# Kernel optimization log

Hardware: AMD Instinct MI355X
Metric: run time of the kernel (lower is better)

Reference implementation:

```python
import jax, jax.numpy as jnp
import numpy as np
import math

D_EMBED = 1024
N_HEADS = 16
HEAD_DIM = D_EMBED // N_HEADS
ROPE_BASE = 10000.0


def apply_rope(x):
    # x: [B, S, H, D] ; torchtune-style interleaved RoPE
    B, S, H, D = x.shape
    half = D // 2
    inv_freq = 1.0 / (ROPE_BASE ** (jnp.arange(0, D, 2, dtype=jnp.float32) / D))  # [half]
    angles = jnp.arange(S, dtype=jnp.float32)[:, None] * inv_freq[None, :]        # [S, half]
    cos = jnp.cos(angles)[None, :, None, :].astype(x.dtype)  # [1,S,1,half]
    sin = jnp.sin(angles)[None, :, None, :].astype(x.dtype)
    x1 = x[..., 0::2]
    x2 = x[..., 1::2]
    o1 = x1 * cos - x2 * sin
    o2 = x1 * sin + x2 * cos
    return jnp.stack([o1, o2], axis=-1).reshape(B, S, H, D)


def setup_inputs() -> dict:
    key = jax.random.key(0)
    ks = jax.random.split(key, 7)
    B, S = 4, 2048
    d_tri = D_EMBED
    q = jax.random.normal(ks[0], (B, S, 2 * d_tri), dtype=jnp.float32)
    k = jax.random.normal(ks[1], (B, S, 2 * d_tri), dtype=jnp.float32)
    v = jax.random.normal(ks[2], (B, S, d_tri), dtype=jnp.float32)
    s_in = 1.0 / math.sqrt(2 * d_tri)
    s_tri = 1.0 / math.sqrt(d_tri)
    W_q = jax.random.normal(ks[3], (D_EMBED, 2 * d_tri), dtype=jnp.float32) * s_in
    W_k = jax.random.normal(ks[4], (D_EMBED, 2 * d_tri), dtype=jnp.float32) * s_in
    W_v = jax.random.normal(ks[5], (d_tri, d_tri), dtype=jnp.float32) * s_tri
    W_o = jax.random.normal(ks[6], (d_tri, d_tri), dtype=jnp.float32) * s_tri
    return {"q": q, "k": k, "v": v, "W_q": W_q, "W_k": W_k, "W_v": W_v, "W_o": W_o}


def reference(q, k, v, W_q, W_k, W_v, W_o):
    B, S, _ = q.shape
    H, Dh = N_HEADS, HEAD_DIM
    scale = 1.0 / math.sqrt(D_EMBED)

    qp = (q @ W_q.T).reshape(B, S, H, Dh)
    kp = (k @ W_k.T).reshape(B, S, H, Dh)
    vp = (v @ W_v.T).reshape(B, S, H, Dh)

    qp = apply_rope(qp)
    kp = apply_rope(kp)

    # [B,H,S,S]
    scores = jnp.einsum('bqhd,bkhd->bhqk', qp, kp) * scale
    causal = jnp.tril(jnp.ones((S, S), dtype=bool))
    scores = jnp.where(causal[None, None], scores, -jnp.inf)
    probs = jax.nn.softmax(scores, axis=-1)
    # dropout layers are identity in eval mode
    out = jnp.einsum('bhqk,bkhd->bqhd', probs, vp).reshape(B, S, D_EMBED)
    return out @ W_o.T
```

## Files before the change

### kernel.cpp

```cpp
#include <hip/hip_runtime.h>
#include <math.h>

#define S_LEN 2048
#define DEMB  1024
#define DH    64

typedef short bf16x8 __attribute__((ext_vector_type(8)));
typedef short bf16x4 __attribute__((ext_vector_type(4)));
typedef float floatx4 __attribute__((ext_vector_type(4)));

__device__ __forceinline__ short f2bf(float f) {
    unsigned u = __builtin_bit_cast(unsigned, f);
    u += 0x7FFFu + ((u >> 16) & 1u);
    return (short)(u >> 16);
}

__global__ void rope_table_k(float2* __restrict__ tab) {
    int idx = blockIdx.x * 256 + threadIdx.x;
    int s = idx >> 5, i = idx & 31;
    double ang = (double)s * pow(10000.0, -(double)i / 32.0);
    tab[idx] = make_float2((float)cos(ang), (float)sin(ang));
}

struct CvtArgs { const float* src[7]; short* dst[7]; int n[7]; };
__global__ __launch_bounds__(256) void cvt_k(CvtArgs a) {
    int seg = blockIdx.y;
    int idx = (blockIdx.x * 256 + threadIdx.x) * 8;
    if (idx >= a.n[seg]) return;
    const float4* s = (const float4*)(a.src[seg] + idx);
    float4 v0 = s[0], v1 = s[1];
    bf16x8 r;
    r[0] = f2bf(v0.x); r[1] = f2bf(v0.y); r[2] = f2bf(v0.z); r[3] = f2bf(v0.w);
    r[4] = f2bf(v1.x); r[5] = f2bf(v1.y); r[6] = f2bf(v1.z); r[7] = f2bf(v1.w);
    *(bf16x8*)(a.dst[seg] + idx) = r;
}

__device__ __forceinline__ void gld16(const void* g, void* l) {
    __builtin_amdgcn_global_load_lds(
        (const __attribute__((address_space(1))) void*)g,
        (__attribute__((address_space(3))) void*)l, 16, 0, 0);
}

template<int EPI>
__device__ __forceinline__ void gemm_body(
    const short* __restrict__ A, const short* __restrict__ B,
    void* __restrict__ Cout, const float2* __restrict__ rope_tab,
    int K, short* smem)
{
    short* sA = smem;
    short* sB = smem + 8192;

    const int tid  = threadIdx.x;
    const int lane = tid & 63;
    const int wv   = tid >> 6;
    const int wm   = wv >> 1, wn = wv & 1;
    const int lr   = lane & 15, quad = lane >> 4;
    const int m0   = blockIdx.y * 128, n0 = blockIdx.x * 128;
    const int N    = 1024;

    const short* gA[4]; const short* gB[4];
    #pragma unroll
    for (int j = 0; j < 4; j++) {
        int c = j * 256 + tid;
        int row = c >> 3, sp = c & 7;
        int cs = (sp ^ (row & 7)) * 8;
        gA[j] = A + (size_t)(m0 + row) * K + cs;
        gB[j] = B + (size_t)(n0 + row) * K + cs;
    }

    floatx4 acc[4][4] = {};

    for (int k0 = 0; k0 < K; k0 += 64) {
        #pragma unroll
        for (int j = 0; j < 4; j++) {
            gld16(gA[j] + k0, sA + j * 2048 + wv * 512);
            gld16(gB[j] + k0, sB + j * 2048 + wv * 512);
        }
        __syncthreads();
        bf16x8 af[4][2], bfr[4][2];
        #pragma unroll
        for (int t = 0; t < 4; t++)
            #pragma unroll
            for (int ks = 0; ks < 2; ks++) {
                int ph = (ks * 4 + quad) ^ (lr & 7);
                af[t][ks]  = *reinterpret_cast<const bf16x8*>(&sA[(wm * 64 + t * 16 + lr) * 64 + ph * 8]);
                bfr[t][ks] = *reinterpret_cast<const bf16x8*>(&sB[(wn * 64 + t * 16 + lr) * 64 + ph * 8]);
            }
        #pragma unroll
        for (int ks = 0; ks < 2; ks++)
            #pragma unroll
            for (int mt = 0; mt < 4; mt++)
                #pragma unroll
                for (int nt = 0; nt < 4; nt++)
                    acc[mt][nt] = __builtin_amdgcn_mfma_f32_16x16x32_bf16(af[mt][ks], bfr[nt][ks], acc[mt][nt], 0, 0, 0);
        __syncthreads();
    }

    if constexpr (EPI == 0) {
        unsigned* sTi = (unsigned*)smem;
        #pragma unroll
        for (int nt = 0; nt < 4; nt++) {
            int n_l = wn * 64 + nt * 16 + lr;
            int ii  = ((n0 + n_l) & 63) >> 1;
            #pragma unroll
            for (int mt = 0; mt < 4; mt++)
                #pragma unroll
                for (int r = 0; r < 4; r++) {
                    int row_l = wm * 64 + mt * 16 + quad * 4 + r;
                    float2 cs = rope_tab[((m0 + row_l) & (S_LEN - 1)) * 32 + ii];
                    float v  = acc[mt][nt][r];
                    float vn = __shfl_xor(v, 1);
                    float o0 = v * cs.x - vn * cs.y;
                    float o1 = vn * cs.x + v * cs.y;
                    if (!(lr & 1)) {
                        unsigned pk = (unsigned)(unsigned short)f2bf(o0) |
                                      ((unsigned)(unsigned short)f2bf(o1) << 16);
                        sTi[row_l * 68 + (n_l >> 1)] = pk;
                    }
                }
        }
        __syncthreads();
        short* C = (short*)Cout;
        #pragma unroll
        for (int j = 0; j < 8; j++) {
            int c = j * 256 + tid;
            int row = c >> 4, col = (c & 15) * 8;
            bf16x8 val = *reinterpret_cast<const bf16x8*>(&smem[row * 136 + col]);
            *reinterpret_cast<bf16x8*>(&C[(size_t)(m0 + row) * N + n0 + col]) = val;
        }
    } else if constexpr (EPI == 2) {
        float* C = (float*)Cout;
        #pragma unroll
        for (int mt = 0; mt < 4; mt++)
            #pragma unroll
            for (int r = 0; r < 4; r++) {
                size_t rowoff = (size_t)(m0 + wm * 64 + mt * 16 + quad * 4 + r) * N;
                #pragma unroll
                for (int nt = 0; nt < 4; nt++)
                    C[rowoff + n0 + wn * 64 + nt * 16 + lr] = acc[mt][nt][r];
            }
    } else {
        short* sT = smem;
        #pragma unroll
        for (int nt = 0; nt < 4; nt++) {
            int nl = wn * 64 + nt * 16 + lr;
            #pragma unroll
            for (int mt = 0; mt < 4; mt++)
                #pragma unroll
                for (int r = 0; r < 4; r++)
                    sT[nl * 136 + wm * 64 + mt * 16 + quad * 4 + r] = f2bf(acc[mt][nt][r]);
        }
        __syncthreads();
        short* C = (short*)Cout;
        int bb = m0 >> 11;
        int s_base = m0 & (S_LEN - 1);
        #pragma unroll
        for (int i = 0; i < 8; i++) {
            int col = (tid >> 4) + i * 16;
            int mc  = (tid & 15) * 8;
            bf16x8 v = *reinterpret_cast<const bf16x8*>(&sT[col * 136 + mc]);
            size_t row = (size_t)bb * DEMB + (n0 + col);
            *reinterpret_cast<bf16x8*>(&C[row * S_LEN + s_base + mc]) = v;
        }
    }
}

__global__ __launch_bounds__(256, 3) void gemm_proj(
    const short* __restrict__ Aq, const short* __restrict__ Bq, void* __restrict__ Cq,
    const short* __restrict__ Ak, const short* __restrict__ Bk, void* __restrict__ Ck,
    const short* __restrict__ Av, const short* __restrict__ Bv, void* __restrict__ Cv,
    const float2* __restrict__ rope_tab)
{
    __shared__ __align__(16) short smem[17408];
    if (blockIdx.z == 0)
        gemm_body<0>(Aq, Bq, Cq, rope_tab, 2048, smem);
    else if (blockIdx.z == 1)
        gemm_body<0>(Ak, Bk, Ck, rope_tab, 2048, smem);
    else
        gemm_body<1>(Av, Bv, Cv, nullptr, 1024, smem);
}

__global__ __launch_bounds__(256, 3) void gemm_out(
    const short* __restrict__ A, const short* __restrict__ B, void* __restrict__ Cout)
{
    __shared__ __align__(16) short smem[17408];
    gemm_body<2>(A, B, Cout, nullptr, 1024, smem);
}

__global__ __launch_bounds__(256, 3) void flash_k(
    const short* __restrict__ qp, const short* __restrict__ kp,
    const short* __restrict__ vpT, short* __restrict__ attn)
{
    __shared__ __align__(16) short sKV[2][2][4096];
    __shared__ __align__(16) short sPb[4][2048];

    const int tid = threadIdx.x;
    const int w = tid >> 6, lane = tid & 63, lr = lane & 15, quad = lane >> 4;
    const int qt = 15 - (blockIdx.x >> 6);
    const int bh = blockIdx.x & 63;
    const int b = bh >> 4, h = bh & 15;
    const int R = qt * 128 + w * 32;
    const size_t qbase = (size_t)(b * S_LEN) * DEMB + h * DH;

    const short* kbase = kp + qbase;
    const short* vbase = vpT + ((size_t)(b * DEMB) + h * DH) * S_LEN;

    const int srow = tid >> 3;
    const int sp   = tid & 7;
    const int cs   = (sp ^ (srow & 7)) * 8;
    short* dK0 = &sKV[0][0][w * 512];  short* dV0 = &sKV[0][1][w * 512];
    short* dK1 = &sKV[1][0][w * 512];  short* dV1 = &sKV[1][1][w * 512];

    bf16x8 qf[2][2];
    #pragma unroll
    for (int mt = 0; mt < 2; mt++)
        #pragma unroll
        for (int ks = 0; ks < 2; ks++)
            qf[mt][ks] = *reinterpret_cast<const bf16x8*>(
                &qp[qbase + (size_t)(R + mt * 16 + lr) * DEMB + ks * 32 + quad * 8]);

    floatx4 oacc[2][4] = {};
    float lsum[2][4] = {};
    const float CEXP = 0.045084220081510574f;
    short* pw = sPb[w];

    const int ktend = 2 * qt + 1;

    auto stage = [&](int kt, int buf) {
        const short* kg = kbase + (size_t)kt * 64 * DEMB;
        const short* vg = vbase + kt * 64;
        short* dK = buf ? dK1 : dK0;
        short* dV = buf ? dV1 : dV0;
        gld16(kg + (size_t)srow * DEMB + cs,        dK);
        gld16(kg + (size_t)(srow + 32) * DEMB + cs, dK + 2048);
        gld16(vg + (size_t)srow * S_LEN + cs,       dV);
        gld16(vg + (size_t)(srow + 32) * S_LEN + cs, dV + 2048);
    };

    stage(0, 0);
    __syncthreads();

    for (int kt = 0; kt <= ktend; kt++) {
        const int cur = kt & 1;
        if (kt < ktend) stage(kt + 1, cur ^ 1);

        if (R + 31 >= kt * 64) {
            const short* sK = sKV[cur][0];
            const short* sV = sKV[cur][1];

            bf16x8 kf[4][2], vf[4][2];
            #pragma unroll
            for (int nt = 0; nt < 4; nt++)
                #pragma unroll
                for (int ks = 0; ks < 2; ks++) {
                    int ph = (ks * 4 + quad) ^ (lr & 7);
                    kf[nt][ks] = *reinterpret_cast<const bf16x8*>(&sK[(nt * 16 + lr) * 64 + ph * 8]);
                    vf[nt][ks] = *reinterpret_cast<const bf16x8*>(&sV[(nt * 16 + lr) * 64 + ph * 8]);
                }

            floatx4 st[2][4];
            #pragma unroll
            for (int nt = 0; nt < 4; nt++)
                #pragma unroll
                for (int mt = 0; mt < 2; mt++) {
                    floatx4 z = {};
                    z = __builtin_amdgcn_mfma_f32_16x16x32_bf16(qf[mt][0], kf[nt][0], z, 0, 0, 0);
                    st[mt][nt] = __builtin_amdgcn_mfma_f32_16x16x32_bf16(qf[mt][1], kf[nt][1], z, 0, 0, 0);
                }

            const bool need_mask = (kt * 64 + 63 > R);
            #pragma unroll
            for (int mt = 0; mt < 2; mt++)
                #pragma unroll
                for (int nt = 0; nt < 4; nt++)
                    #pragma unroll
                    for (int r = 0; r < 4; r++) {
                        float t = fminf(st[mt][nt][r] * CEXP, 80.f);
                        float p = __builtin_amdgcn_exp2f(t);
                        if (need_mask) {
                            int col = kt * 64 + nt * 16 + lr;
                            int row = R + mt * 16 + quad * 4 + r;
                            p = (col > row) ? 0.f : p;
                        }
                        st[mt][nt][r] = p;
                        lsum[mt][r] += p;
                    }

            #pragma unroll
            for (int mt = 0; mt < 2; mt++)
                #pragma unroll
                for (int nt = 0; nt < 4; nt++)
                    #pragma unroll
                    for (int r = 0; r < 4; r++) {
                        int rw = mt * 16 + quad * 4 + r;
                        int chunk = (nt * 2 + (lr >> 3)) ^ (rw & 7);
                        pw[rw * 64 + chunk * 8 + (lr & 7)] = f2bf(st[mt][nt][r]);
                    }

            bf16x8 pf[2][2];
            #pragma unroll
            for (int mt = 0; mt < 2; mt++)
                #pragma unroll
                for (int ks = 0; ks < 2; ks++) {
                    int rr = mt * 16 + lr;
                    int c  = (ks * 4 + quad) ^ (rr & 7);
                    pf[mt][ks] = *reinterpret_cast<const bf16x8*>(&pw[rr * 64 + c * 8]);
                }

            #pragma unroll
            for (int d = 0; d < 4; d++)
                #pragma unroll
                for (int mt = 0; mt < 2; mt++) {
                    oacc[mt][d] = __builtin_amdgcn_mfma_f32_16x16x32_bf16(pf[mt][0], vf[d][0], oacc[mt][d], 0, 0, 0);
                    oacc[mt][d] = __builtin_amdgcn_mfma_f32_16x16x32_bf16(pf[mt][1], vf[d][1], oacc[mt][d], 0, 0, 0);
                }
        }
        __syncthreads();
    }

    #pragma unroll
    for (int mt = 0; mt < 2; mt++)
        #pragma unroll
        for (int r = 0; r < 4; r++) {
            float l = lsum[mt][r];
            l += __shfl_xor(l, 1);
            l += __shfl_xor(l, 2);
            l += __shfl_xor(l, 4);
            l += __shfl_xor(l, 8);
            float inv = 1.f / l;
            size_t rowoff = qbase + (size_t)(R + mt * 16 + quad * 4 + r) * DEMB;
            #pragma unroll
            for (int d = 0; d < 4; d++)
                attn[rowoff + d * 16 + lr] = f2bf(oacc[mt][d][r] * inv);
        }
}

__device__ __forceinline__ bf16x4 load4(const float* p) {
    const float4 v = *reinterpret_cast<const float4*>(p);
    bf16x4 r; r[0] = f2bf(v.x); r[1] = f2bf(v.y); r[2] = f2bf(v.z); r[3] = f2bf(v.w);
    return r;
}
__device__ __forceinline__ bf16x4 load4(const short* p) {
    return *reinterpret_cast<const bf16x4*>(p);
}

template<typename TA, int EPI>
__global__ __launch_bounds__(256) void gemm_nt(
    const TA* __restrict__ A, const float* __restrict__ B,
    void* __restrict__ Cout, const float2* __restrict__ rope_tab,
    int M, int N, int K)
{
    __shared__ __align__(16) short smem[(EPI == 1) ? (128 * 136) : (2 * 128 * 40)];
    short* sA = smem;
    short* sB = smem + 128 * 40;

    const int tid  = threadIdx.x;
    const int lane = tid & 63;
    const int wv   = tid >> 6;
    const int wm   = wv >> 1, wn = wv & 1;
    const int lr   = lane & 15, quad = lane >> 4;
    const int m0   = blockIdx.y * 128, n0 = blockIdx.x * 128;

    floatx4 acc[4][4] = {};

    for (int k0 = 0; k0 < K; k0 += 32) {
        #pragma unroll
        for (int i = 0; i < 4; i++) {
            int c = tid + i * 256;
            int row = c >> 3, kc = (c & 7) << 2;
            bf16x4 v = load4(&A[(size_t)(m0 + row) * K + k0 + kc]);
            *reinterpret_cast<bf16x4*>(&sA[row * 40 + kc]) = v;
        }
        #pragma unroll
        for (int i = 0; i < 4; i++) {
            int c = tid + i * 256;
            int row = c >> 3, kc = (c & 7) << 2;
            bf16x4 v = load4(&B[(size_t)(n0 + row) * K + k0 + kc]);
            *reinterpret_cast<bf16x4*>(&sB[row * 40 + kc]) = v;
        }
        __syncthreads();
        bf16x8 af[4], bfr[4];
        #pragma unroll
        for (int t = 0; t < 4; t++)
            af[t] = *reinterpret_cast<const bf16x8*>(&sA[(wm * 64 + t * 16 + lr) * 40 + quad * 8]);
        #pragma unroll
        for (int t = 0; t < 4; t++)
            bfr[t] = *reinterpret_cast<const bf16x8*>(&sB[(wn * 64 + t * 16 + lr) * 40 + quad * 8]);
        #pragma unroll
        for (int mt = 0; mt < 4; mt++)
            #pragma unroll
            for (int nt = 0; nt < 4; nt++)
                acc[mt][nt] = __builtin_amdgcn_mfma_f32_16x16x32_bf16(af[mt], bfr[nt], acc[mt][nt], 0, 0, 0);
        __syncthreads();
    }

    if constexpr (EPI == 0) {
        short* C = (short*)Cout;
        #pragma unroll
        for (int nt = 0; nt < 4; nt++) {
            int n_g = n0 + wn * 64 + nt * 16 + lr;
            int ii  = (n_g & 63) >> 1;
            bool evenc = (n_g & 1) == 0;
            #pragma unroll
            for (int mt = 0; mt < 4; mt++) {
                #pragma unroll
                for (int r = 0; r < 4; r++) {
                    int m_g = m0 + wm * 64 + mt * 16 + quad * 4 + r;
                    float2 cs = rope_tab[(m_g & (S_LEN - 1)) * 32 + ii];
                    float v  = acc[mt][nt][r];
                    float vn = __shfl_xor(v, 1);
                    float o = evenc ? (v * cs.x - vn * cs.y) : (v * cs.x + vn * cs.y);
                    C[(size_t)m_g * N + n_g] = f2bf(o);
                }
            }
        }
    } else if constexpr (EPI == 2) {
        float* C = (float*)Cout;
        #pragma unroll
        for (int mt = 0; mt < 4; mt++)
            #pragma unroll
            for (int r = 0; r < 4; r++) {
                size_t rowoff = (size_t)(m0 + wm * 64 + mt * 16 + quad * 4 + r) * N;
                #pragma unroll
                for (int nt = 0; nt < 4; nt++)
                    C[rowoff + n0 + wn * 64 + nt * 16 + lr] = acc[mt][nt][r];
            }
    } else {
        short* sT = smem;
        __syncthreads();
        #pragma unroll
        for (int nt = 0; nt < 4; nt++) {
            int nl = wn * 64 + nt * 16 + lr;
            #pragma unroll
            for (int mt = 0; mt < 4; mt++)
                #pragma unroll
                for (int r = 0; r < 4; r++)
                    sT[nl * 136 + wm * 64 + mt * 16 + quad * 4 + r] = f2bf(acc[mt][nt][r]);
        }
        __syncthreads();
        short* C = (short*)Cout;
        int bb = m0 >> 11;
        int s_base = m0 & (S_LEN - 1);
        #pragma unroll
        for (int i = 0; i < 8; i++) {
            int col = (tid >> 4) + i * 16;
            int mc  = (tid & 15) * 8;
            bf16x8 v = *reinterpret_cast<const bf16x8*>(&sT[col * 136 + mc]);
            size_t row = (size_t)bb * DEMB + (n0 + col);
            *reinterpret_cast<bf16x8*>(&C[row * S_LEN + s_base + mc]) = v;
        }
    }
}

extern "C" void kernel_launch(void* const* d_in, const int* in_sizes, int n_in,
                              void* d_out, int out_size, void* d_ws, size_t ws_size,
                              hipStream_t stream) {
    const float* q  = (const float*)d_in[0];
    const float* k  = (const float*)d_in[1];
    const float* v  = (const float*)d_in[2];
    const float* Wq = (const float*)d_in[3];
    const float* Wk = (const float*)d_in[4];
    const float* Wv = (const float*)d_in[5];
    const float* Wo = (const float*)d_in[6];
    float* out = (float*)d_out;

    char* ws = (char*)d_ws;
    const size_t MB = 1024 * 1024;
    short*  qp   = (short*)(ws);
    short*  kp   = (short*)(ws + 16 * MB);
    short*  vpT  = (short*)(ws + 32 * MB);
    short*  attn = (short*)(ws + 48 * MB);
    float2* tab  = (float2*)(ws + 64 * MB);

    rope_table_k<<<256, 256, 0, stream>>>(tab);

    dim3 g2(8, 64);
    if (ws_size >= 157 * MB) {
        short* qb  = (short*)(ws + 65 * MB);
        short* kb  = (short*)(ws + 97 * MB);
        short* vb  = (short*)(ws + 129 * MB);
        short* wqb = (short*)(ws + 145 * MB);
        short* wkb = (short*)(ws + 149 * MB);
        short* wvb = (short*)(ws + 153 * MB);
        short* wob = (short*)(ws + 155 * MB);

        CvtArgs ca;
        ca.src[0] = q;  ca.dst[0] = qb;  ca.n[0] = 16777216;
        ca.src[1] = k;  ca.dst[1] = kb;  ca.n[1] = 16777216;
        ca.src[2] = v;  ca.dst[2] = vb;  ca.n[2] = 8388608;
        ca.src[3] = Wq; ca.dst[3] = wqb; ca.n[3] = 2097152;
        ca.src[4] = Wk; ca.dst[4] = wkb; ca.n[4] = 2097152;
        ca.src[5] = Wv; ca.dst[5] = wvb; ca.n[5] = 1048576;
        ca.src[6] = Wo; ca.dst[6] = wob; ca.n[6] = 1048576;
        cvt_k<<<dim3(8192, 7), 256, 0, stream>>>(ca);

        gemm_proj<<<dim3(8, 64, 3), 256, 0, stream>>>(
            qb, wqb, qp, kb, wkb, kp, vb, wvb, vpT, tab);
        flash_k<<<1024, 256, 0, stream>>>(qp, kp, vpT, attn);
        gemm_out<<<g2, 256, 0, stream>>>(attn, wob, out);
    } else {
        gemm_nt<float, 0><<<g2, 256, 0, stream>>>(q, Wq, qp,  tab,     8192, 1024, 2048);
        gemm_nt<float, 0><<<g2, 256, 0, stream>>>(k, Wk, kp,  tab,     8192, 1024, 2048);
        gemm_nt<float, 1><<<g2, 256, 0, stream>>>(v, Wv, vpT, nullptr, 8192, 1024, 1024);
        flash_k<<<1024, 256, 0, stream>>>(qp, kp, vpT, attn);
        gemm_nt<short, 2><<<g2, 256, 0, stream>>>(attn, Wo, out, nullptr, 8192, 1024, 1024);
    }
}
```

Baseline: 432.1 us.

## Load K/V fragments directly from global in flash kernel, drop LDS staging

Removes the double-buffered LDS staging of K and V tiles and the per-tile block barrier. Each wave now reads its MFMA K and V fragments straight from global memory and runs only up to its own causal end. Block-to-query-tile mapping is interleaved so heavy and light causal tiles pair within each head, and MFMA phases get raised wave priority. Occupancy target rises to 4 blocks per CU. The risk is redundant global/L2 traffic across the four waves and exposed load latency without prefetch.

```diff
diff --git a/kernel.cpp b/kernel.cpp
--- a/kernel.cpp
+++ b/kernel.cpp
@@ -187,29 +187,24 @@
     gemm_body<2>(A, B, Cout, nullptr, 1024, smem);
 }
 
-__global__ __launch_bounds__(256, 3) void flash_k(
+__global__ __launch_bounds__(256, 4) void flash_k(
     const short* __restrict__ qp, const short* __restrict__ kp,
     const short* __restrict__ vpT, short* __restrict__ attn)
 {
-    __shared__ __align__(16) short sKV[2][2][4096];
     __shared__ __align__(16) short sPb[4][2048];
 
     const int tid = threadIdx.x;
     const int w = tid >> 6, lane = tid & 63, lr = lane & 15, quad = lane >> 4;
-    const int qt = 15 - (blockIdx.x >> 6);
-    const int bh = blockIdx.x & 63;
+    const int bx = blockIdx.x;
+    const int tq = bx & 15;
+    const int qt = (tq < 8) ? (15 - tq) : (tq - 8);
+    const int bh = bx >> 4;
     const int b = bh >> 4, h = bh & 15;
     const int R = qt * 128 + w * 32;
     const size_t qbase = (size_t)(b * S_LEN) * DEMB + h * DH;
 
     const short* kbase = kp + qbase;
     const short* vbase = vpT + ((size_t)(b * DEMB) + h * DH) * S_LEN;
-
-    const int srow = tid >> 3;
-    const int sp   = tid & 7;
-    const int cs   = (sp ^ (srow & 7)) * 8;
-    short* dK0 = &sKV[0][0][w * 512];  short* dV0 = &sKV[0][1][w * 512];
-    short* dK1 = &sKV[1][0][w * 512];  short* dV1 = &sKV[1][1][w * 512];
 
     bf16x8 qf[2][2];
     #pragma unroll
@@ -224,98 +219,84 @@
     const float CEXP = 0.045084220081510574f;
     short* pw = sPb[w];
 
-    const int ktend = 2 * qt + 1;
-
-    auto stage = [&](int kt, int buf) {
-        const short* kg = kbase + (size_t)kt * 64 * DEMB;
-        const short* vg = vbase + kt * 64;
-        short* dK = buf ? dK1 : dK0;
-        short* dV = buf ? dV1 : dV0;
-        gld16(kg + (size_t)srow * DEMB + cs,        dK);
-        gld16(kg + (size_t)(srow + 32) * DEMB + cs, dK + 2048);
-        gld16(vg + (size_t)srow * S_LEN + cs,       dV);
-        gld16(vg + (size_t)(srow + 32) * S_LEN + cs, dV + 2048);
-    };
-
-    stage(0, 0);
-    __syncthreads();
-
-    for (int kt = 0; kt <= ktend; kt++) {
-        const int cur = kt & 1;
-        if (kt < ktend) stage(kt + 1, cur ^ 1);
-
-        if (R + 31 >= kt * 64) {
-            const short* sK = sKV[cur][0];
-            const short* sV = sKV[cur][1];
-
-            bf16x8 kf[4][2], vf[4][2];
+    const int myend = (R + 31) >> 6;
+
+    for (int kt = 0; kt <= myend; kt++) {
+        const short* kT = kbase + (size_t)kt * 64 * DEMB;
+        const short* vT = vbase + kt * 64;
+
+        floatx4 st[2][4];
+        __builtin_amdgcn_s_setprio(1);
+        #pragma unroll
+        for (int nt = 0; nt < 4; nt++) {
+            const short* kr = kT + (size_t)(nt * 16 + lr) * DEMB + quad * 8;
+            bf16x8 kf0 = *reinterpret_cast<const bf16x8*>(kr);
+            bf16x8 kf1 = *reinterpret_cast<const bf16x8*>(kr + 32);
+            #pragma unroll
+            for (int mt = 0; mt < 2; mt++) {
+                floatx4 z = {};
+                z = __builtin_amdgcn_mfma_f32_16x16x32_bf16(qf[mt][0], kf0, z, 0, 0, 0);
+                st[mt][nt] = __builtin_amdgcn_mfma_f32_16x16x32_bf16(qf[mt][1], kf1, z, 0, 0, 0);
+            }
+        }
+        __builtin_amdgcn_s_setprio(0);
+
+        const bool need_mask = (kt * 64 + 63 > R);
+        #pragma unroll
+        for (int mt = 0; mt < 2; mt++)
             #pragma unroll
             for (int nt = 0; nt < 4; nt++)
                 #pragma unroll
-                for (int ks = 0; ks < 2; ks++) {
-                    int ph = (ks * 4 + quad) ^ (lr & 7);
-                    kf[nt][ks] = *reinterpret_cast<const bf16x8*>(&sK[(nt * 16 + lr) * 64 + ph * 8]);
-                    vf[nt][ks] = *reinterpret_cast<const bf16x8*>(&sV[(nt * 16 + lr) * 64 + ph * 8]);
+                for (int r = 0; r < 4; r++) {
+                    float t = fminf(st[mt][nt][r] * CEXP, 80.f);
+                    float p = __builtin_amdgcn_exp2f(t);
+                    if (need_mask) {
+                        int col = kt * 64 + nt * 16 + lr;
+                        int row = R + mt * 16 + quad * 4 + r;
+                        p = (col > row) ? 0.f : p;
+                    }
+                    st[mt][nt][r] = p;
+                    lsum[mt][r] += p;
                 }
 
-            floatx4 st[2][4];
+        bf16x8 vf[4][2];
+        #pragma unroll
+        for (int d = 0; d < 4; d++) {
+            const short* vr = vT + (size_t)(d * 16 + lr) * S_LEN + quad * 8;
+            vf[d][0] = *reinterpret_cast<const bf16x8*>(vr);
+            vf[d][1] = *reinterpret_cast<const bf16x8*>(vr + 32);
+        }
+
+        #pragma unroll
+        for (int mt = 0; mt < 2; mt++)
             #pragma unroll
             for (int nt = 0; nt < 4; nt++)
                 #pragma unroll
-                for (int mt = 0; mt < 2; mt++) {
-                    floatx4 z = {};
-                    z = __builtin_amdgcn_mfma_f32_16x16x32_bf16(qf[mt][0], kf[nt][0], z, 0, 0, 0);
-                    st[mt][nt] = __builtin_amdgcn_mfma_f32_16x16x32_bf16(qf[mt][1], kf[nt][1], z, 0, 0, 0);
+                for (int r = 0; r < 4; r++) {
+                    int rw = mt * 16 + quad * 4 + r;
+                    int chunk = (nt * 2 + (lr >> 3)) ^ (rw & 7);
+                    pw[rw * 64 + chunk * 8 + (lr & 7)] = f2bf(st[mt][nt][r]);
                 }
 
-            const bool need_mask = (kt * 64 + 63 > R);
-            #pragma unroll
-            for (int mt = 0; mt < 2; mt++)
-                #pragma unroll
-                for (int nt = 0; nt < 4; nt++)
-                    #pragma unroll
-                    for (int r = 0; r < 4; r++) {
-                        float t = fminf(st[mt][nt][r] * CEXP, 80.f);
-                        float p = __builtin_amdgcn_exp2f(t);
-                        if (need_mask) {
-                            int col = kt * 64 + nt * 16 + lr;
-                            int row = R + mt * 16 + quad * 4 + r;
-                            p = (col > row) ? 0.f : p;
-                        }
-                        st[mt][nt][r] = p;
-                        lsum[mt][r] += p;
-                    }
-
-            #pragma unroll
-            for (int mt = 0; mt < 2; mt++)
-                #pragma unroll
-                for (int nt = 0; nt < 4; nt++)
-                    #pragma unroll
-                    for (int r = 0; r < 4; r++) {
-                        int rw = mt * 16 + quad * 4 + r;
-                        int chunk = (nt * 2 + (lr >> 3)) ^ (rw & 7);
-                        pw[rw * 64 + chunk * 8 + (lr & 7)] = f2bf(st[mt][nt][r]);
-                    }
-
-            bf16x8 pf[2][2];
-            #pragma unroll
-            for (int mt = 0; mt < 2; mt++)
-                #pragma unroll
-                for (int ks = 0; ks < 2; ks++) {
-                    int rr = mt * 16 + lr;
-                    int c  = (ks * 4 + quad) ^ (rr & 7);
-                    pf[mt][ks] = *reinterpret_cast<const bf16x8*>(&pw[rr * 64 + c * 8]);
-                }
-
-            #pragma unroll
-            for (int d = 0; d < 4; d++)
-                #pragma unroll
-                for (int mt = 0; mt < 2; mt++) {
-                    oacc[mt][d] = __builtin_amdgcn_mfma_f32_16x16x32_bf16(pf[mt][0], vf[d][0], oacc[mt][d], 0, 0, 0);
-                    oacc[mt][d] = __builtin_amdgcn_mfma_f32_16x16x32_bf16(pf[mt][1], vf[d][1], oacc[mt][d], 0, 0, 0);
-                }
-        }
-        __syncthreads();
+        bf16x8 pf[2][2];
+        #pragma unroll
+        for (int mt = 0; mt < 2; mt++)
+            #pragma unroll
+            for (int ks = 0; ks < 2; ks++) {
+                int rr = mt * 16 + lr;
+                int c  = (ks * 4 + quad) ^ (rr & 7);
+                pf[mt][ks] = *reinterpret_cast<const bf16x8*>(&pw[rr * 64 + c * 8]);
+            }
+
+        __builtin_amdgcn_s_setprio(1);
+        #pragma unroll
+        for (int d = 0; d < 4; d++)
+            #pragma unroll
+            for (int mt = 0; mt < 2; mt++) {
+                oacc[mt][d] = __builtin_amdgcn_mfma_f32_16x16x32_bf16(pf[mt][0], vf[d][0], oacc[mt][d], 0, 0, 0);
+                oacc[mt][d] = __builtin_amdgcn_mfma_f32_16x16x32_bf16(pf[mt][1], vf[d][1], oacc[mt][d], 0, 0, 0);
+            }
+        __builtin_amdgcn_s_setprio(0);
     }
 
     #pragma unroll
```

New measurement: 759.7 us. 1.76x slower.
